# Optimization experiments

Measured on AMD Instinct MI355X. Metric: run time of the kernel, lower is better.

The kernel has to match this reference:

```python
import jax, jax.numpy as jnp
import numpy as np

B, N_HEADS, D_MODEL, S = 4, 16, 128, 2048
SQRT_D = np.sqrt(D_MODEL).astype(np.float32)


def setup_inputs() -> dict:
    key = jax.random.key(0)
    kx, kq, kk, kv, kw = jax.random.split(key, 5)
    N = B * N_HEADS
    return {
        "x": jax.random.normal(kx, (B, D_MODEL, S), dtype=jnp.float32),
        "Q": jax.random.normal(kq, (N, D_MODEL, S), dtype=jnp.float32),
        "K": jax.random.normal(kk, (N, D_MODEL, S), dtype=jnp.float32),
        "V": jax.random.normal(kv, (N, D_MODEL, S), dtype=jnp.float32),
        "W": jax.random.normal(kw, (N_HEADS * D_MODEL, D_MODEL), dtype=jnp.float32) * 0.02,
    }


def reference(x, Q, K, V, W):
    # x contributes only its shape (the repeated copy is overwritten in the original)
    b, d_model, s = x.shape
    # scores[n, i, j] = sum_d Q[n, d, i] * K[n, d, j] / sqrt(d_model)
    scores = jnp.einsum("ndi,ndj->nij", Q, K) / SQRT_D  # [N, S, S]
    # legacy F.softmax (no dim) on a 3D tensor -> softmax over dim=1 (query index)
    attn = jax.nn.softmax(scores, axis=1)
    # out[n, d, j] = sum_i V[n, d, i] * attn[n, i, j]
    out = jnp.einsum("ndi,nij->ndj", V, attn)  # [N, d_model, S]
    out = out.reshape(b, N_HEADS * d_model, s)  # [B, H*d_model, S]
    # final projection: W^T @ out, W: [H*d_model, d_model]
    return jnp.einsum("hd,bhs->bds", W, out)  # [B, d_model, S]
```

## Files before the change

### kernel.cpp

```cpp
#include <hip/hip_runtime.h>
#include <hip/hip_bf16.h>

typedef unsigned short u16;
typedef unsigned int   u32;
typedef short  short8v __attribute__((ext_vector_type(8)));
typedef u16    u16x8   __attribute__((ext_vector_type(8)));
typedef float  f32x16  __attribute__((ext_vector_type(16)));
typedef float  f32x4v  __attribute__((ext_vector_type(4)));
typedef u32    u32x2   __attribute__((ext_vector_type(2)));
typedef u32    u32x4   __attribute__((ext_vector_type(4)));

#define HEADS 64
#define DMODEL 128
#define SEQ 2048

#define SCQ 0.1275293f


__device__ __forceinline__ f32x16 mfma_bf16(short8v a, short8v b, f32x16 c) {
  return __builtin_amdgcn_mfma_f32_32x32x16_bf16(a, b, c, 0, 0, 0);
}

__device__ __forceinline__ f32x16 fzero16() {
  f32x16 z;
#pragma unroll
  for (int i = 0; i < 16; ++i) z[i] = 0.f;
  return z;
}

__device__ __forceinline__ float fast_exp2(float x) {
  float r;
  asm("v_exp_f32 %0, %1" : "=v"(r) : "v"(x));
  return r;
}

__device__ __forceinline__ u32 bfround(float x) {
  u32 u = __builtin_bit_cast(u32, x);
  u += 0x7fffu + ((u >> 16) & 1u);
  return u >> 16;
}
__device__ __forceinline__ u32 bfpair(float lo, float hi) {
  u32 a = __builtin_bit_cast(u32, lo); a += 0x7fffu + ((a >> 16) & 1u);
  u32 b = __builtin_bit_cast(u32, hi); b += 0x7fffu + ((b >> 16) & 1u);
  return (a >> 16) | (b & 0xffff0000u);
}
__device__ __forceinline__ u32 packbf(float lo, float hi) {
  u32 l16 = (u32)__builtin_bit_cast(u16, __float2bfloat16(lo));
  u32 h16 = (u32)__builtin_bit_cast(u16, __float2bfloat16(hi));
  return l16 | (h16 << 16);
}

typedef const __attribute__((address_space(1))) void* gp1_t;
typedef __attribute__((address_space(3))) void* lp3_t;
__device__ __forceinline__ void gload16(const u16* g, u16* l) {
  __builtin_amdgcn_global_load_lds((gp1_t)g, (lp3_t)l, 16, 0, 0);
}

__device__ __forceinline__ void stage_T(const float* __restrict__ src, int pos0,
                                        u16* lds, int tid) {
  int ic = tid & 7;
  int d0 = (tid >> 3) * 2;
  const float* p = src + d0 * SEQ + pos0 + ic * 8;
  f32x4v xa = *reinterpret_cast<const f32x4v*>(p);
  f32x4v xb = *reinterpret_cast<const f32x4v*>(p + 4);
  f32x4v ya = *reinterpret_cast<const f32x4v*>(p + SEQ);
  f32x4v yb = *reinterpret_cast<const f32x4v*>(p + SEQ + 4);
  u32* lds32 = reinterpret_cast<u32*>(lds);
  int cc = d0 >> 3;
#pragma unroll
  for (int k = 0; k < 8; ++k) {
    int r = ic * 8 + k;
    int c2 = cc ^ (r & 15);
    float xv = (k < 4) ? xa[k & 3] : xb[k & 3];
    float yv = (k < 4) ? ya[k & 3] : yb[k & 3];
    lds32[(r * 128 + c2 * 8 + (d0 & 7)) >> 1] = bfpair(xv, yv);
  }
}

__device__ __forceinline__ short8v ld_at(const u16* lds, int row, int chunk) {
  return *reinterpret_cast<const short8v*>(lds + row * 128 + ((chunk ^ (row & 15)) * 8));
}
__device__ __forceinline__ short8v ld_vt(const u16* lds, int d, int chunk) {
  return *reinterpret_cast<const short8v*>(lds + d * 64 + ((chunk ^ (d & 7)) * 8));
}


__global__ __launch_bounds__(256) void prep_qt(const float* __restrict__ Q,
                                               u16* __restrict__ Qt) {
  int blk = blockIdx.x;
  int n = blk >> 5, pt = blk & 31;
  const float* src = Q + (size_t)n * DMODEL * SEQ;
  u16* dst = Qt + (size_t)n * SEQ * DMODEL + (size_t)pt * 64 * DMODEL;
  int t = threadIdx.x;
  int pq = t & 15, dq = t >> 4;
#pragma unroll
  for (int p = 0; p < 2; ++p) {
    int d0 = (dq + 16 * p) * 4;
    const float* s0 = src + (size_t)d0 * SEQ + pt * 64 + pq * 4;
    f32x4v r0 = *reinterpret_cast<const f32x4v*>(s0);
    f32x4v r1 = *reinterpret_cast<const f32x4v*>(s0 + SEQ);
    f32x4v r2 = *reinterpret_cast<const f32x4v*>(s0 + 2 * SEQ);
    f32x4v r3 = *reinterpret_cast<const f32x4v*>(s0 + 3 * SEQ);
#pragma unroll
    for (int j = 0; j < 4; ++j) {
      u32x2 v = { bfpair(r0[j] * SCQ, r1[j] * SCQ), bfpair(r2[j] * SCQ, r3[j] * SCQ) };
      *reinterpret_cast<u32x2*>(dst + (pq * 4 + j) * DMODEL + d0) = v;
    }
  }
}

__global__ __launch_bounds__(256) void prep_v(const float* __restrict__ V,
                                              u16* __restrict__ V16t) {
  int blk = blockIdx.x;
  int n = blk >> 5, it = blk & 31;
  int t = threadIdx.x;
  int s8 = (t & 7) * 8;
  const float* src = V + (size_t)n * DMODEL * SEQ + it * 64 + s8;
  u16* dst = V16t + (size_t)blk * DMODEL * 64 + s8;
#pragma unroll
  for (int rr = 0; rr < 4; ++rr) {
    int d = (t >> 3) + 32 * rr;
    const float* p = src + (size_t)d * SEQ;
    f32x4v a = *reinterpret_cast<const f32x4v*>(p);
    f32x4v b = *reinterpret_cast<const f32x4v*>(p + 4);
    u32x4 v = { bfpair(a[0], a[1]), bfpair(a[2], a[3]),
                bfpair(b[0], b[1]), bfpair(b[2], b[3]) };
    *reinterpret_cast<u32x4*>(dst + d * 64) = v;
  }
}

__global__ void wtrans_kernel(const float* __restrict__ Wsrc, u16* __restrict__ Wt) {
  int e = blockIdx.x * 256 + threadIdx.x;
#pragma unroll
  for (int rr = 0; rr < 2; ++rr) {
    int o = e + rr * 131072;
    int dm = o >> 11, c = o & 2047;
    Wt[o] = (u16)bfround(Wsrc[c * 128 + dm]);
  }
}

#define BUFW (64 * 128 + 128 * 64)

__global__ __launch_bounds__(512, 2) void attn_kernel(
    const u16* __restrict__ Qt, const float* __restrict__ K,
    const u16* __restrict__ V16t, u16* __restrict__ Ows) {
  __shared__ __align__(16) u16 LDSb[4 * BUFW];
  const int tid = threadIdx.x;
  const int w = tid >> 6;
  const int lane = tid & 63;
  const int g = lane >> 5;
  const int lj = lane & 31;
  const int p_ = blockIdx.x;
  const int n = ((p_ >> 6) << 3) | (p_ & 7);
  const int j0 = ((p_ >> 3) & 7) * 256;
  const u16* Qtn = Qt + (size_t)n * SEQ * DMODEL;
  const float* Kb = K + (size_t)n * DMODEL * SEQ;
  const u16* Vtn = V16t + (size_t)n * 32 * DMODEL * 64;

  int qoff[4], voff[4];
#pragma unroll
  for (int i = 0; i < 4; ++i) {
    int idx = (w & 3) * 4 + i;
    int pos = idx * 4 + (lane >> 4);
    qoff[i] = pos * DMODEL + (((lane & 15) ^ (pos & 15)) * 8);
    int d = idx * 8 + (lane >> 3);
    voff[i] = d * 64 + (((lane & 7) ^ (d & 7)) * 8);
  }

#define ISSUE_TILE(tile, buf)                                              \
  {                                                                        \
    if (w < 4) {                                                           \
      const u16* qb = Qtn + (size_t)(tile) * (64 * DMODEL);                \
      _Pragma("unroll") for (int i = 0; i < 4; ++i)                        \
          gload16(qb + qoff[i], (buf) + ((w & 3) * 4 + i) * 512);          \
    } else {                                                               \
      const u16* vb = Vtn + (size_t)(tile) * (DMODEL * 64);                \
      _Pragma("unroll") for (int i = 0; i < 4; ++i)                        \
          gload16(vb + voff[i], (buf) + 64 * DMODEL + ((w & 3) * 4 + i) * 512); \
    }                                                                      \
  }

  short8v bq[8];
#pragma unroll 1
  for (int p = 0; p < 4; ++p) {
    stage_T(Kb, j0 + p * 64, LDSb, tid);
    __syncthreads();
    if ((w >> 1) == p) {
      int row = (w & 1) * 32 + lj;
#pragma unroll
      for (int c = 0; c < 8; ++c) bq[c] = ld_at(LDSb, row, 2 * c + g);
    }
    __syncthreads();
  }

  ISSUE_TILE(0, LDSb);
  ISSUE_TILE(1, LDSb + BUFW);
  asm volatile("s_waitcnt vmcnt(0)" ::: "memory");
  __builtin_amdgcn_s_barrier();

  f32x16 o0 = fzero16(), o1 = fzero16(), o2 = fzero16(), o3 = fzero16();
  float m_run = -1e30f, l_run = 0.f;

#pragma unroll 1
  for (int ss = 0; ss < 16; ++ss) {
    u16* cp = LDSb + (ss & 1) * (2 * BUFW);
    u16* op = LDSb + ((ss & 1) ^ 1) * (2 * BUFW);

    ISSUE_TILE((2 * ss + 2) & 31, op);
    ISSUE_TILE((2 * ss + 3) & 31, op + BUFW);

#pragma unroll
    for (int h = 0; h < 2; ++h) {
      u16* curAT = cp + h * BUFW;
      u16* curVT = curAT + 64 * DMODEL;

      f32x16 c0 = fzero16(), c1 = fzero16();
      __builtin_amdgcn_s_setprio(1);
#pragma unroll
      for (int dc = 0; dc < 8; ++dc) {
        short8v a0 = ld_at(curAT, lj, 2 * dc + g);
        short8v a1 = ld_at(curAT, 32 + lj, 2 * dc + g);
        c0 = mfma_bf16(a0, bq[dc], c0);
        c1 = mfma_bf16(a1, bq[dc], c1);
      }
      __builtin_amdgcn_s_setprio(0);

      float m8[8];
#pragma unroll
      for (int r = 0; r < 8; ++r)
        m8[r] = fmaxf(fmaxf(c0[r], c0[r + 8]), fmaxf(c1[r], c1[r + 8]));
#pragma unroll
      for (int r = 0; r < 4; ++r) m8[r] = fmaxf(m8[r], m8[r + 4]);
      float mx = fmaxf(fmaxf(m8[0], m8[1]), fmaxf(m8[2], m8[3]));
      mx = fmaxf(mx, __shfl_xor(mx, 32, 64));

      if (!__all(mx <= m_run + 8.f)) {
        float mn = fmaxf(m_run, mx);
        float al = fast_exp2(m_run - mn);
        m_run = mn;
        l_run *= al;
#pragma unroll
        for (int r = 0; r < 16; ++r) { o0[r] *= al; o1[r] *= al; o2[r] *= al; o3[r] *= al; }
      }
#pragma unroll
      for (int r = 0; r < 16; ++r) c0[r] = fast_exp2(c0[r] - m_run);
#pragma unroll
      for (int r = 0; r < 16; ++r) c1[r] = fast_exp2(c1[r] - m_run);
      float s8[8];
#pragma unroll
      for (int r = 0; r < 8; ++r) s8[r] = (c0[r] + c0[r + 8]) + (c1[r] + c1[r + 8]);
#pragma unroll
      for (int r = 0; r < 4; ++r) s8[r] += s8[r + 4];
      float ps = (s8[0] + s8[1]) + (s8[2] + s8[3]);
      ps += __shfl_xor(ps, 32, 64);
      l_run += ps;

      u32 pk[8], ok[8];
#pragma unroll
      for (int half = 0; half < 2; ++half) {
#pragma unroll
        for (int q = 0; q < 4; ++q) {
#pragma unroll
          for (int hh = 0; hh < 2; ++hh) {
            float va = half ? c1[q * 4 + 2 * hh]     : c0[q * 4 + 2 * hh];
            float vb = half ? c1[q * 4 + 2 * hh + 1] : c0[q * 4 + 2 * hh + 1];
            pk[q * 2 + hh] = packbf(va, vb);
          }
        }
#pragma unroll
        for (int i = 0; i < 8; ++i) ok[i] = __shfl_xor(pk[i], 32, 64);
        __builtin_amdgcn_s_setprio(1);
#pragma unroll
        for (int kh = 0; kh < 2; ++kh) {
          int kc = half * 2 + kh;
          const int base = 4 * kh;
          u32 w0 = g ? ok[base + 2] : pk[base + 0];
          u32 w1 = g ? ok[base + 3] : pk[base + 1];
          u32 w2 = g ? pk[base + 2] : ok[base + 0];
          u32 w3 = g ? pk[base + 3] : ok[base + 1];
          u32x4 uu = {w0, w1, w2, w3};
          short8v pf = __builtin_bit_cast(short8v, uu);
          short8v v0 = ld_vt(curVT, lj,      2 * kc + g);
          short8v v1 = ld_vt(curVT, 32 + lj, 2 * kc + g);
          short8v v2 = ld_vt(curVT, 64 + lj, 2 * kc + g);
          short8v v3 = ld_vt(curVT, 96 + lj, 2 * kc + g);
          o0 = mfma_bf16(v0, pf, o0);
          o1 = mfma_bf16(v1, pf, o1);
          o2 = mfma_bf16(v2, pf, o2);
          o3 = mfma_bf16(v3, pf, o3);
        }
        __builtin_amdgcn_s_setprio(0);
      }
    }

    asm volatile("s_waitcnt vmcnt(0)" ::: "memory");
    __builtin_amdgcn_sched_barrier(0);
    __builtin_amdgcn_s_barrier();
    __builtin_amdgcn_sched_barrier(0);
  }

  float inv = 1.f / l_run;
  int jme = j0 + w * 32 + lj;
  u16* obase = Ows + ((size_t)n * SEQ + jme) * DMODEL;

#define STORE_OT(OV, DT)                                                  \
  {                                                                       \
    _Pragma("unroll") for (int q = 0; q < 4; ++q) {                       \
      int d0 = (DT) * 32 + 4 * g + 8 * q;                                 \
      u32x2 val;                                                          \
      val.x = bfpair(OV[4 * q + 0] * inv, OV[4 * q + 1] * inv);           \
      val.y = bfpair(OV[4 * q + 2] * inv, OV[4 * q + 3] * inv);           \
      *reinterpret_cast<u32x2*>(obase + d0) = val;                        \
    }                                                                     \
  }
  STORE_OT(o0, 0) STORE_OT(o1, 1) STORE_OT(o2, 2) STORE_OT(o3, 3)
#undef STORE_OT
#undef ISSUE_TILE
}

__global__ __launch_bounds__(256) void proj_kernel(
    const u16* __restrict__ Ows, const u16* __restrict__ Wt, float* __restrict__ out) {
  __shared__ __align__(16) u16 BT[32 * 128];
  const int tid = threadIdx.x;
  const int w = tid >> 6, lane = tid & 63, g = lane >> 5, lj = lane & 31;
  const int b = blockIdx.x >> 6;
  const int j0 = (blockIdx.x & 63) * 32;
  f32x16 acc = fzero16();
#pragma unroll 1
  for (int h = 0; h < 16; ++h) {
    __syncthreads();
#pragma unroll
    for (int rr = 0; rr < 2; ++rr) {
      int s = tid + rr * 256;
      int r = s >> 4, cc = s & 15;
      u16x8 v = *reinterpret_cast<const u16x8*>(
          Ows + ((size_t)(b * 16 + h) * SEQ + j0 + r) * DMODEL + cc * 8);
      *reinterpret_cast<u16x8*>(BT + r * 128 + ((cc ^ (r & 7)) * 8)) = v;
    }
    __syncthreads();
#pragma unroll
    for (int kc = 0; kc < 8; ++kc) {
      short8v a = *reinterpret_cast<const short8v*>(
          Wt + (size_t)(w * 32 + lj) * SEQ + h * 128 + kc * 16 + g * 8);
      short8v bb = *reinterpret_cast<const short8v*>(
          BT + lj * 128 + (((2 * kc + g) ^ (lj & 7)) * 8));
      acc = mfma_bf16(a, bb, acc);
    }
  }
#pragma unroll
  for (int q = 0; q < 4; ++q) {
#pragma unroll
    for (int r = 0; r < 4; ++r) {
      int dm = w * 32 + 4 * g + 8 * q + r;
      out[((size_t)b * DMODEL + dm) * SEQ + j0 + lj] = acc[4 * q + r];
    }
  }
}

extern "C" void kernel_launch(void* const* d_in, const int* in_sizes, int n_in,
                              void* d_out, int out_size, void* d_ws, size_t ws_size,
                              hipStream_t stream) {
  (void)in_sizes; (void)n_in; (void)out_size; (void)ws_size;
  const float* Q = (const float*)d_in[1];
  const float* K = (const float*)d_in[2];
  const float* V = (const float*)d_in[3];
  const float* W = (const float*)d_in[4];
  const size_t NEL = (size_t)HEADS * SEQ * DMODEL;
  u16* Qt   = (u16*)d_ws;
  u16* V16t = Qt + NEL;
  u16* Ows  = V16t + NEL;
  u16* Wt   = Ows + NEL;
  float* out = (float*)d_out;

  prep_qt<<<dim3(2048), dim3(256), 0, stream>>>(Q, Qt);
  prep_v<<<dim3(2048), dim3(256), 0, stream>>>(V, V16t);
  wtrans_kernel<<<dim3(512), dim3(256), 0, stream>>>(W, Wt);
  attn_kernel<<<dim3(512), dim3(512), 0, stream>>>(Qt, K, V16t, Ows);
  proj_kernel<<<dim3(256), dim3(256), 0, stream>>>(Ows, Wt, out);
}
```

Measured before the change: 243.1 us.

## Split attention into producer softmax waves and consumer PV waves via LDS

```diff
diff --git a/kernel.cpp b/kernel.cpp
--- a/kernel.cpp
+++ b/kernel.cpp
@@ -139,12 +139,14 @@
   }
 }
 
-#define BUFW (64 * 128 + 128 * 64)
-
-__global__ __launch_bounds__(512, 2) void attn_kernel(
+__global__ __launch_bounds__(1024, 4) void attn_kernel(
     const u16* __restrict__ Qt, const float* __restrict__ K,
     const u16* __restrict__ V16t, u16* __restrict__ Ows) {
-  __shared__ __align__(16) u16 LDSb[4 * BUFW];
+  __shared__ __align__(16) u16 AT2[2][64 * DMODEL];
+  __shared__ __align__(16) u16 VT2[2][DMODEL * 64];
+  __shared__ __align__(16) u16 PB[2][256 * 64];
+  __shared__ float AL[2][256];
+  __shared__ float LL[256];
   const int tid = threadIdx.x;
   const int w = tid >> 6;
   const int lane = tid & 63;
@@ -157,129 +159,142 @@
   const float* Kb = K + (size_t)n * DMODEL * SEQ;
   const u16* Vtn = V16t + (size_t)n * 32 * DMODEL * 64;
 
-  int qoff[4], voff[4];
-#pragma unroll
-  for (int i = 0; i < 4; ++i) {
-    int idx = (w & 3) * 4 + i;
+  int qoff[2], voff[2];
+#pragma unroll
+  for (int i = 0; i < 2; ++i) {
+    int idx = (w & 7) * 2 + i;
     int pos = idx * 4 + (lane >> 4);
     qoff[i] = pos * DMODEL + (((lane & 15) ^ (pos & 15)) * 8);
     int d = idx * 8 + (lane >> 3);
     voff[i] = d * 64 + (((lane & 7) ^ (d & 7)) * 8);
   }
 
-#define ISSUE_TILE(tile, buf)                                              \
-  {                                                                        \
-    if (w < 4) {                                                           \
-      const u16* qb = Qtn + (size_t)(tile) * (64 * DMODEL);                \
-      _Pragma("unroll") for (int i = 0; i < 4; ++i)                        \
-          gload16(qb + qoff[i], (buf) + ((w & 3) * 4 + i) * 512);          \
-    } else {                                                               \
-      const u16* vb = Vtn + (size_t)(tile) * (DMODEL * 64);                \
-      _Pragma("unroll") for (int i = 0; i < 4; ++i)                        \
-          gload16(vb + voff[i], (buf) + 64 * DMODEL + ((w & 3) * 4 + i) * 512); \
-    }                                                                      \
-  }
-
+  if (w < 8) {
+    const u16* qb = Qtn;
+#pragma unroll
+    for (int i = 0; i < 2; ++i)
+      gload16(qb + qoff[i], AT2[0] + ((w & 7) * 2 + i) * 512);
+  }
   short8v bq[8];
+  u16* KS = PB[0];
 #pragma unroll 1
   for (int p = 0; p < 4; ++p) {
-    stage_T(Kb, j0 + p * 64, LDSb, tid);
-    __syncthreads();
-    if ((w >> 1) == p) {
+    if (tid < 512) stage_T(Kb, j0 + p * 64, KS, tid);
+    __syncthreads();
+    if (w < 8 && (w >> 1) == p) {
       int row = (w & 1) * 32 + lj;
 #pragma unroll
-      for (int c = 0; c < 8; ++c) bq[c] = ld_at(LDSb, row, 2 * c + g);
-    }
-    __syncthreads();
-  }
-
-  ISSUE_TILE(0, LDSb);
-  ISSUE_TILE(1, LDSb + BUFW);
-  asm volatile("s_waitcnt vmcnt(0)" ::: "memory");
-  __builtin_amdgcn_s_barrier();
-
-  f32x16 o0 = fzero16(), o1 = fzero16(), o2 = fzero16(), o3 = fzero16();
-  float m_run = -1e30f, l_run = 0.f;
+      for (int c = 0; c < 8; ++c) bq[c] = ld_at(KS, row, 2 * c + g);
+    }
+    __syncthreads();
+  }
+
+  if (w < 8) {
+    float m_run = -1e30f, l_run = 0.f;
+    const int prow = w * 32 + lj;
+    u16* const prowbase0 = PB[0] + prow * 64;
+    u16* const prowbase1 = PB[1] + prow * 64;
+    const int swz = prow & 7;
 
 #pragma unroll 1
-  for (int ss = 0; ss < 16; ++ss) {
-    u16* cp = LDSb + (ss & 1) * (2 * BUFW);
-    u16* op = LDSb + ((ss & 1) ^ 1) * (2 * BUFW);
-
-    ISSUE_TILE((2 * ss + 2) & 31, op);
-    ISSUE_TILE((2 * ss + 3) & 31, op + BUFW);
-
-#pragma unroll
-    for (int h = 0; h < 2; ++h) {
-      u16* curAT = cp + h * BUFW;
-      u16* curVT = curAT + 64 * DMODEL;
-
-      f32x16 c0 = fzero16(), c1 = fzero16();
-      __builtin_amdgcn_s_setprio(1);
-#pragma unroll
-      for (int dc = 0; dc < 8; ++dc) {
-        short8v a0 = ld_at(curAT, lj, 2 * dc + g);
-        short8v a1 = ld_at(curAT, 32 + lj, 2 * dc + g);
-        c0 = mfma_bf16(a0, bq[dc], c0);
-        c1 = mfma_bf16(a1, bq[dc], c1);
+    for (int t = 0; t <= 32; ++t) {
+      if (t < 32) {
+        const u16* qb = Qtn + (size_t)((t + 1) & 31) * (64 * DMODEL);
+        u16* ab = AT2[(t + 1) & 1];
+#pragma unroll
+        for (int i = 0; i < 2; ++i)
+          gload16(qb + qoff[i], ab + ((w & 7) * 2 + i) * 512);
+
+        const u16* curAT = AT2[t & 1];
+        f32x16 c0 = fzero16(), c1 = fzero16();
+        __builtin_amdgcn_s_setprio(1);
+#pragma unroll
+        for (int dc = 0; dc < 8; ++dc) {
+          short8v a0 = ld_at(curAT, lj, 2 * dc + g);
+          short8v a1 = ld_at(curAT, 32 + lj, 2 * dc + g);
+          c0 = mfma_bf16(a0, bq[dc], c0);
+          c1 = mfma_bf16(a1, bq[dc], c1);
+        }
+        __builtin_amdgcn_s_setprio(0);
+
+        float m8[8];
+#pragma unroll
+        for (int r = 0; r < 8; ++r)
+          m8[r] = fmaxf(fmaxf(c0[r], c0[r + 8]), fmaxf(c1[r], c1[r + 8]));
+#pragma unroll
+        for (int r = 0; r < 4; ++r) m8[r] = fmaxf(m8[r], m8[r + 4]);
+        float mx = fmaxf(fmaxf(m8[0], m8[1]), fmaxf(m8[2], m8[3]));
+        mx = fmaxf(mx, __shfl_xor(mx, 32, 64));
+
+        float al = 1.0f;
+        if (!__all(mx <= m_run + 8.f)) {
+          float mn = fmaxf(m_run, mx);
+          al = fast_exp2(m_run - mn);
+          m_run = mn;
+          l_run *= al;
+        }
+        if (!g) AL[t & 1][prow] = al;
+
+#pragma unroll
+        for (int r = 0; r < 16; ++r) c0[r] = fast_exp2(c0[r] - m_run);
+#pragma unroll
+        for (int r = 0; r < 16; ++r) c1[r] = fast_exp2(c1[r] - m_run);
+        float s8[8];
+#pragma unroll
+        for (int r = 0; r < 8; ++r) s8[r] = (c0[r] + c0[r + 8]) + (c1[r] + c1[r + 8]);
+#pragma unroll
+        for (int r = 0; r < 4; ++r) s8[r] += s8[r + 4];
+        float ps = (s8[0] + s8[1]) + (s8[2] + s8[3]);
+        ps += __shfl_xor(ps, 32, 64);
+        l_run += ps;
+
+        u16* pdst = (t & 1) ? prowbase1 : prowbase0;
+#pragma unroll
+        for (int half = 0; half < 2; ++half) {
+#pragma unroll
+          for (int q = 0; q < 4; ++q) {
+            u32x2 val;
+            val.x = half ? packbf(c1[4 * q + 0], c1[4 * q + 1])
+                         : packbf(c0[4 * q + 0], c0[4 * q + 1]);
+            val.y = half ? packbf(c1[4 * q + 2], c1[4 * q + 3])
+                         : packbf(c0[4 * q + 2], c0[4 * q + 3]);
+            int G = q + 4 * half;
+            *reinterpret_cast<u32x2*>(pdst + ((G ^ swz) << 3) + 4 * g) = val;
+          }
+        }
       }
-      __builtin_amdgcn_s_setprio(0);
-
-      float m8[8];
-#pragma unroll
-      for (int r = 0; r < 8; ++r)
-        m8[r] = fmaxf(fmaxf(c0[r], c0[r + 8]), fmaxf(c1[r], c1[r + 8]));
-#pragma unroll
-      for (int r = 0; r < 4; ++r) m8[r] = fmaxf(m8[r], m8[r + 4]);
-      float mx = fmaxf(fmaxf(m8[0], m8[1]), fmaxf(m8[2], m8[3]));
-      mx = fmaxf(mx, __shfl_xor(mx, 32, 64));
-
-      if (!__all(mx <= m_run + 8.f)) {
-        float mn = fmaxf(m_run, mx);
-        float al = fast_exp2(m_run - mn);
-        m_run = mn;
-        l_run *= al;
-#pragma unroll
-        for (int r = 0; r < 16; ++r) { o0[r] *= al; o1[r] *= al; o2[r] *= al; o3[r] *= al; }
+      __syncthreads();
+    }
+    if (!g) LL[prow] = l_run;
+    __syncthreads();
+  } else {
+    f32x16 o0 = fzero16(), o1 = fzero16(), o2 = fzero16(), o3 = fzero16();
+    const int prow = (w - 8) * 32 + lj;
+    const int swz = prow & 7;
+
+#pragma unroll 1
+    for (int t = 0; t <= 32; ++t) {
+      if (t < 32) {
+        const u16* vb = Vtn + (size_t)t * (DMODEL * 64);
+        u16* vbuf = VT2[t & 1];
+#pragma unroll
+        for (int i = 0; i < 2; ++i)
+          gload16(vb + voff[i], vbuf + ((w & 7) * 2 + i) * 512);
       }
-#pragma unroll
-      for (int r = 0; r < 16; ++r) c0[r] = fast_exp2(c0[r] - m_run);
-#pragma unroll
-      for (int r = 0; r < 16; ++r) c1[r] = fast_exp2(c1[r] - m_run);
-      float s8[8];
-#pragma unroll
-      for (int r = 0; r < 8; ++r) s8[r] = (c0[r] + c0[r + 8]) + (c1[r] + c1[r + 8]);
-#pragma unroll
-      for (int r = 0; r < 4; ++r) s8[r] += s8[r + 4];
-      float ps = (s8[0] + s8[1]) + (s8[2] + s8[3]);
-      ps += __shfl_xor(ps, 32, 64);
-      l_run += ps;
-
-      u32 pk[8], ok[8];
-#pragma unroll
-      for (int half = 0; half < 2; ++half) {
-#pragma unroll
-        for (int q = 0; q < 4; ++q) {
-#pragma unroll
-          for (int hh = 0; hh < 2; ++hh) {
-            float va = half ? c1[q * 4 + 2 * hh]     : c0[q * 4 + 2 * hh];
-            float vb = half ? c1[q * 4 + 2 * hh + 1] : c0[q * 4 + 2 * hh + 1];
-            pk[q * 2 + hh] = packbf(va, vb);
-          }
-        }
-#pragma unroll
-        for (int i = 0; i < 8; ++i) ok[i] = __shfl_xor(pk[i], 32, 64);
+      if (t >= 1) {
+        const int tp = t - 1;
+        const u16* curVT = VT2[tp & 1];
+        const u16* prowp = PB[tp & 1] + prow * 64;
+        float al = AL[tp & 1][prow];
+        if (!__all(al == 1.0f)) {
+#pragma unroll
+          for (int r = 0; r < 16; ++r) { o0[r] *= al; o1[r] *= al; o2[r] *= al; o3[r] *= al; }
+        }
         __builtin_amdgcn_s_setprio(1);
 #pragma unroll
-        for (int kh = 0; kh < 2; ++kh) {
-          int kc = half * 2 + kh;
-          const int base = 4 * kh;
-          u32 w0 = g ? ok[base + 2] : pk[base + 0];
-          u32 w1 = g ? ok[base + 3] : pk[base + 1];
-          u32 w2 = g ? pk[base + 2] : ok[base + 0];
-          u32 w3 = g ? pk[base + 3] : ok[base + 1];
-          u32x4 uu = {w0, w1, w2, w3};
-          short8v pf = __builtin_bit_cast(short8v, uu);
+        for (int kc = 0; kc < 4; ++kc) {
+          short8v pf = *reinterpret_cast<const short8v*>(
+              prowp + (((2 * kc + g) ^ swz) << 3));
           short8v v0 = ld_vt(curVT, lj,      2 * kc + g);
           short8v v1 = ld_vt(curVT, 32 + lj, 2 * kc + g);
           short8v v2 = ld_vt(curVT, 64 + lj, 2 * kc + g);
@@ -291,31 +306,25 @@
         }
         __builtin_amdgcn_s_setprio(0);
       }
-    }
-
-    asm volatile("s_waitcnt vmcnt(0)" ::: "memory");
-    __builtin_amdgcn_sched_barrier(0);
-    __builtin_amdgcn_s_barrier();
-    __builtin_amdgcn_sched_barrier(0);
-  }
-
-  float inv = 1.f / l_run;
-  int jme = j0 + w * 32 + lj;
-  u16* obase = Ows + ((size_t)n * SEQ + jme) * DMODEL;
-
+      __syncthreads();
+    }
+    __syncthreads();
+    float inv = 1.f / LL[prow];
+    int jme = j0 + prow;
+    u16* obase = Ows + ((size_t)n * SEQ + jme) * DMODEL;
 #define STORE_OT(OV, DT)                                                  \
-  {                                                                       \
-    _Pragma("unroll") for (int q = 0; q < 4; ++q) {                       \
-      int d0 = (DT) * 32 + 4 * g + 8 * q;                                 \
-      u32x2 val;                                                          \
-      val.x = bfpair(OV[4 * q + 0] * inv, OV[4 * q + 1] * inv);           \
-      val.y = bfpair(OV[4 * q + 2] * inv, OV[4 * q + 3] * inv);           \
-      *reinterpret_cast<u32x2*>(obase + d0) = val;                        \
-    }                                                                     \
-  }
-  STORE_OT(o0, 0) STORE_OT(o1, 1) STORE_OT(o2, 2) STORE_OT(o3, 3)
+    {                                                                     \
+      _Pragma("unroll") for (int q = 0; q < 4; ++q) {                     \
+        int d0 = (DT) * 32 + 4 * g + 8 * q;                               \
+        u32x2 val;                                                        \
+        val.x = bfpair(OV[4 * q + 0] * inv, OV[4 * q + 1] * inv);         \
+        val.y = bfpair(OV[4 * q + 2] * inv, OV[4 * q + 3] * inv);         \
+        *reinterpret_cast<u32x2*>(obase + d0) = val;                      \
+      }                                                                   \
+    }
+    STORE_OT(o0, 0) STORE_OT(o1, 1) STORE_OT(o2, 2) STORE_OT(o3, 3)
 #undef STORE_OT
-#undef ISSUE_TILE
+  }
 }
 
 __global__ __launch_bounds__(256) void proj_kernel(
@@ -375,6 +384,6 @@
   prep_qt<<<dim3(2048), dim3(256), 0, stream>>>(Q, Qt);
   prep_v<<<dim3(2048), dim3(256), 0, stream>>>(V, V16t);
   wtrans_kernel<<<dim3(512), dim3(256), 0, stream>>>(W, Wt);
-  attn_kernel<<<dim3(512), dim3(512), 0, stream>>>(Qt, K, V16t, Ows);
+  attn_kernel<<<dim3(512), dim3(1024), 0, stream>>>(Qt, K, V16t, Ows);
   proj_kernel<<<dim3(256), dim3(256), 0, stream>>>(Ows, Wt, out);
 }
```

After: 238.5 us. No clear change (-1.9%).
